# Optimization experiments

Hardware: AMD Instinct MI355X
Metric: run time of the kernel (lower is better)

The kernel has to match this reference:

```python
import jax, jax.numpy as jnp
import numpy as np

B, CIN, COUT, H, W = 32, 64, 64, 58, 58
RSIZE, NB, EDIM = 512, 10, 64


def setup_inputs() -> dict:
    key = jax.random.key(0)
    ks = jax.random.split(key, 8)
    return {
        "x": jax.random.normal(ks[0], (B, CIN, H, W), jnp.float32),
        "routing_vector": jax.random.normal(ks[1], (B, RSIZE), jnp.float32),
        "W1": jax.random.normal(ks[2], (RSIZE, 128), jnp.float32) * 0.02,
        "b1": jnp.zeros((128,), jnp.float32),
        "W2": jax.random.normal(ks[3], (128, EDIM), jnp.float32) * 0.05,
        "b2": jnp.zeros((EDIM,), jnp.float32),
        "emb": jax.random.normal(ks[4], (NB, EDIM), jnp.float32),
        "conv_w": jax.random.normal(ks[5], (NB, COUT, CIN, 3, 3), jnp.float32) * 0.02,
        "conv_b": jnp.zeros((NB, COUT), jnp.float32),
    }


def _cosine_similarity(a, b):
    # calculate_similarity assumed cosine: [B,E] x [N,E] -> [B,N]
    a = a / (jnp.linalg.norm(a, axis=-1, keepdims=True) + 1e-8)
    b = b / (jnp.linalg.norm(b, axis=-1, keepdims=True) + 1e-8)
    return a @ b.T


def reference(x, routing_vector, W1, b1, W2, b2, emb, conv_w, conv_b):
    # process_routing: Linear(512,128) -> ReLU -> Linear(128,64)
    r = jax.nn.relu(routing_vector @ W1 + b1) @ W2 + b2          # [B, 64]
    sim = _cosine_similarity(r, emb)                              # [B, NB]
    # eval mode: no noise; SIMPLESampler treated as identity on softmax weights
    weights = jax.nn.softmax(sim, axis=-1)                        # [B, NB]
    # run all NB expert convs as one valid 3x3 conv with NB*COUT output channels
    w_all = conv_w.reshape(NB * COUT, CIN, 3, 3)
    y = jax.lax.conv_general_dilated(
        x, w_all, window_strides=(1, 1), padding='VALID',
        dimension_numbers=('NCHW', 'OIHW', 'NCHW'))               # [B, NB*COUT, 56, 56]
    y = y + conv_b.reshape(1, NB * COUT, 1, 1)
    y = y.reshape(B, NB, COUT, y.shape[-2], y.shape[-1])          # [B, NB, COUT, 56, 56]
    # weighted mixture over experts; softmax weights sum to 1 (d in torch code)
    d = jnp.sum(weights, axis=-1)                                 # [B]
    out = jnp.einsum('bnchw,bn->bchw', y, weights) / d[:, None, None, None]
    return out
```

## Files before the change

### kernel.cpp

```cpp
#include <hip/hip_runtime.h>
#include <hip/hip_bf16.h>
#include <stdint.h>

#define BATCH 32
#define CIN   64
#define COUT  64
#define HIN   58
#define WIN   58
#define HOUT  56
#define WOUT  56
#define RSIZE 512
#define NB    10
#define EDIM  64
#define HID   128
#define CHW   (HIN*WIN)
#define OHW   (HOUT*WOUT)

typedef __attribute__((ext_vector_type(8)))  short short8;
typedef __attribute__((ext_vector_type(16))) float f32x16;

__device__ __forceinline__ unsigned short f2bf(float f) {
    unsigned int u = __builtin_bit_cast(unsigned int, f);
    u += 0x7fffu + ((u >> 16) & 1u);
    return (unsigned short)(u >> 16);
}

__global__ __launch_bounds__(512) void route_kernel(
    const float* __restrict__ rv, const float* __restrict__ W1,
    const float* __restrict__ b1, const float* __restrict__ W2,
    const float* __restrict__ b2, const float* __restrict__ emb,
    float* __restrict__ wts)
{
    const int b = blockIdx.x;
    const int t = threadIdx.x;

    __shared__ float s_rv[RSIZE];
    __shared__ float s_part[4 * HID];
    __shared__ float s_h[HID];
    __shared__ float s_r[EDIM];
    __shared__ float s_rn;
    __shared__ float s_sim[NB];

    if (t < 128) ((float4*)s_rv)[t] = ((const float4*)(rv + (size_t)b * RSIZE))[t];
    __syncthreads();

    {
        const int h = t & 127, kq = t >> 7;
        float acc = 0.0f;
        const float* wp = W1 + (size_t)(kq * 128) * HID + h;
        const float* xp = s_rv + kq * 128;
        #pragma unroll 8
        for (int k = 0; k < 128; ++k) acc = fmaf(xp[k], wp[(size_t)k * HID], acc);
        s_part[kq * HID + h] = acc;
    }
    __syncthreads();
    if (t < HID)
        s_h[t] = fmaxf(s_part[t] + s_part[HID + t] + s_part[2 * HID + t] +
                       s_part[3 * HID + t] + b1[t], 0.0f);
    __syncthreads();

    {
        const int e = t & 63, kq = t >> 6;
        float acc = 0.0f;
        const float* wp = W2 + (size_t)(kq * 16) * EDIM + e;
        const float* hp = s_h + kq * 16;
        #pragma unroll
        for (int k = 0; k < 16; ++k) acc = fmaf(hp[k], wp[(size_t)k * EDIM], acc);
        s_part[kq * 64 + e] = acc;
    }
    __syncthreads();
    if (t < EDIM) {
        float r = b2[t];
        #pragma unroll
        for (int q = 0; q < 8; ++q) r += s_part[q * 64 + t];
        s_r[t] = r;
    }
    __syncthreads();

    if (t < 64) {
        float sq = s_r[t] * s_r[t];
        #pragma unroll
        for (int off = 32; off; off >>= 1) sq += __shfl_xor(sq, off);
        if (t == 0) s_rn = sqrtf(sq);
    }
    __syncthreads();

    {
        const int wid = t >> 6, lane = t & 63;
        for (int n = wid; n < NB; n += 8) {
            const float ev = emb[n * EDIM + lane];
            float dot = ev * s_r[lane];
            float nb2 = ev * ev;
            #pragma unroll
            for (int off = 32; off; off >>= 1) {
                dot += __shfl_xor(dot, off);
                nb2 += __shfl_xor(nb2, off);
            }
            if (lane == 0)
                s_sim[n] = dot / ((s_rn + 1e-8f) * (sqrtf(nb2) + 1e-8f));
        }
    }
    __syncthreads();

    if (t == 0) {
        float m = -1e30f;
        #pragma unroll
        for (int n = 0; n < NB; ++n) m = fmaxf(m, s_sim[n]);
        float w[NB], sum = 0.0f;
        #pragma unroll
        for (int n = 0; n < NB; ++n) { w[n] = __expf(s_sim[n] - m); sum += w[n]; }
        const float inv = 1.0f / sum;
        float d = 0.0f;
        #pragma unroll
        for (int n = 0; n < NB; ++n) { w[n] *= inv; d += w[n]; }
        const float invd = 1.0f / d;
        #pragma unroll
        for (int n = 0; n < NB; ++n) wts[b * NB + n] = w[n] * invd;
    }
}

__global__ __launch_bounds__(256) void wmix2_kernel(
    const float* __restrict__ cw, const float* __restrict__ cbias,
    const float* __restrict__ wts,
    unsigned short* __restrict__ weffb, float* __restrict__ sbias_g)
{
    const int co = blockIdx.x & 63;
    const int bq = blockIdx.x >> 6;
    const int t  = threadIdx.x;

    __shared__ float scw[NB * 576];
    __shared__ float s_w[8 * NB];

    if (t < 8 * NB) s_w[t] = wts[bq * 8 * NB + t];
    for (int i = t; i < 1440; i += 256) {
        const int n = i / 144, r4 = i - n * 144;
        ((float4*)scw)[(size_t)n * 144 + r4] =
            *(const float4*)(cw + (size_t)(n * COUT + co) * 576 + r4 * 4);
    }
    __syncthreads();

    for (int i = t; i < 8 * 576; i += 256) {
        const int bl  = i / 576, rem = i - bl * 576;
        const int s   = rem >> 6, cin = rem & 63;
        float v = 0.0f;
        #pragma unroll
        for (int n = 0; n < NB; ++n)
            v = fmaf(s_w[bl * NB + n], scw[n * 576 + cin * 9 + s], v);
        const int b  = bq * 8 + bl;
        const int ks = cin >> 4, kg = (cin >> 3) & 1, c8 = cin & 7;
        weffb[((((size_t)(b * 9 + s) * 4 + ks) * 2 + kg) * 64 + co) * 8 + c8] = f2bf(v);
    }
    if (t < 8) {
        float v = 0.0f;
        #pragma unroll
        for (int n = 0; n < NB; ++n) v = fmaf(s_w[t * NB + n], cbias[n * COUT + co], v);
        sbias_g[(bq * 8 + t) * COUT + co] = v;
    }
}

__global__ __launch_bounds__(256, 2) void conv4_kernel(
    const float* __restrict__ x, const unsigned short* __restrict__ weffb,
    const float* __restrict__ sbias_g, float* __restrict__ out)
{
    const int bid  = blockIdx.x;
    const int xcd  = bid & 7;
    const int slot = bid >> 3;
    const int b    = xcd + 8 * (slot / 28);
    const int tile = slot - (slot / 28) * 28;
    const int oh0  = tile * 2;

    const int t    = threadIdx.x;
    const int wid  = t >> 6;
    const int lane = t & 63;
    const int ln   = lane & 31;
    const int kg   = lane >> 5;
    const int mt   = wid & 1;
    const int nh   = wid >> 1;

    __shared__ unsigned short xs[232 * 64];
    __shared__ float sbias[COUT];

    if (t < COUT) sbias[t] = sbias_g[b * COUT + t];

    const float* xg = x + (size_t)b * CIN * CHW + oh0 * WIN;
    #pragma unroll
    for (int k = 0; k < 8; ++k) {
        const int e = t + 256 * k;
        if (e < 1856) {
            const int cb = e / 232;
            const int sp = e - cb * 232;
            const float* gp = xg + (size_t)(cb * 8) * CHW + sp;
            short8 v;
            #pragma unroll
            for (int j = 0; j < 8; ++j)
                v[j] = (short)f2bf(gp[(size_t)j * CHW]);
            *(short8*)&xs[sp * 64 + (cb ^ (sp & 7)) * 8] = v;
        }
    }
    __syncthreads();

    int sbase[2]; int pq[2]; bool val[2];
    #pragma unroll
    for (int nt = 0; nt < 2; ++nt) {
        const int p = (nh * 2 + nt) * 32 + ln;
        val[nt] = (p < 112);
        const int pc = val[nt] ? p : 111;
        pq[nt] = pc;
        const int r = pc / 56, ow = pc - r * 56;
        sbase[nt] = r * WIN + ow;
    }

    f32x16 acc[2];
    #pragma unroll
    for (int nt = 0; nt < 2; ++nt)
        #pragma unroll
        for (int j = 0; j < 16; ++j) acc[nt][j] = 0.0f;

    const unsigned short* abase =
        weffb + (size_t)b * 36864 + kg * 512 + (mt * 32 + ln) * 8;

    #pragma unroll
    for (int ks = 0; ks < 4; ++ks) {
        short8 af[9];
        #pragma unroll
        for (int s = 0; s < 9; ++s)
            af[s] = *(const short8*)(abase + (size_t)s * 4096 + ks * 1024);

        #pragma unroll
        for (int s = 0; s < 9; ++s) {
            const int kh = s / 3, kw = s - kh * 3;
            const int off = kh * WIN + kw;
            #pragma unroll
            for (int nt = 0; nt < 2; ++nt) {
                const int sp   = sbase[nt] + off;
                const int addr = (sp << 7) + ((((ks << 1) + kg) ^ (sp & 7)) << 4);
                const short8 bf = *(const short8*)((const char*)xs + addr);
                acc[nt] = __builtin_amdgcn_mfma_f32_32x32x16_bf16(af[s], bf, acc[nt], 0, 0, 0);
            }
        }
    }

    #pragma unroll
    for (int nt = 0; nt < 2; ++nt) {
        if (!val[nt]) continue;
        const int p = pq[nt];
        const int r = p / 56, ow = p - r * 56;
        float* op = out + ((size_t)(b * COUT + mt * 32) * HOUT + oh0 + r) * WOUT + ow;
        #pragma unroll
        for (int reg = 0; reg < 16; ++reg) {
            const int co_l = (reg & 3) + 8 * (reg >> 2) + 4 * kg;
            op[(size_t)co_l * OHW] = acc[nt][reg] + sbias[mt * 32 + co_l];
        }
    }
}

extern "C" void kernel_launch(void* const* d_in, const int* in_sizes, int n_in,
                              void* d_out, int out_size, void* d_ws, size_t ws_size,
                              hipStream_t stream) {
    const float* x    = (const float*)d_in[0];
    const float* rv   = (const float*)d_in[1];
    const float* W1   = (const float*)d_in[2];
    const float* b1   = (const float*)d_in[3];
    const float* W2   = (const float*)d_in[4];
    const float* b2   = (const float*)d_in[5];
    const float* emb  = (const float*)d_in[6];
    const float* cw   = (const float*)d_in[7];
    const float* cb   = (const float*)d_in[8];
    float* out = (float*)d_out;

    float* wts            = (float*)d_ws;
    float* sbias_g        = (float*)d_ws + 1024;
    unsigned short* weffb = (unsigned short*)((float*)d_ws + 3072);

    route_kernel<<<dim3(BATCH), dim3(512), 0, stream>>>(rv, W1, b1, W2, b2, emb, wts);
    wmix2_kernel<<<dim3(256), dim3(256), 0, stream>>>(cw, cb, wts, weffb, sbias_g);
    conv4_kernel<<<dim3(BATCH * 28), dim3(256), 0, stream>>>(x, weffb, sbias_g, out);
}
```

Baseline: 39.54 us.

## Split conv input staging into two channel halves and use direct-to-LDS loads in weight mix

The conv kernel now stages the input tile in two 32-channel halves with a smaller LDS buffer and a new swizzle, and raises the occupancy hint to 4 blocks per SM. This is meant to let more blocks run at once and hide global load latency. The cost is an extra barrier phase, and the input staging is now serialized with the MFMA work within each block. The weight-mix kernel switches to 512 threads and uses global_load_lds to copy conv weights straight into LDS, avoiding the register round trip.

```diff
diff --git a/kernel.cpp b/kernel.cpp
--- a/kernel.cpp
+++ b/kernel.cpp
@@ -119,7 +119,7 @@
     }
 }
 
-__global__ __launch_bounds__(256) void wmix2_kernel(
+__global__ __launch_bounds__(512) void wmix2b_kernel(
     const float* __restrict__ cw, const float* __restrict__ cbias,
     const float* __restrict__ wts,
     unsigned short* __restrict__ weffb, float* __restrict__ sbias_g)
@@ -132,14 +132,25 @@
     __shared__ float s_w[8 * NB];
 
     if (t < 8 * NB) s_w[t] = wts[bq * 8 * NB + t];
-    for (int i = t; i < 1440; i += 256) {
-        const int n = i / 144, r4 = i - n * 144;
-        ((float4*)scw)[(size_t)n * 144 + r4] =
-            *(const float4*)(cw + (size_t)(n * COUT + co) * 576 + r4 * 4);
-    }
-    __syncthreads();
-
-    for (int i = t; i < 8 * 576; i += 256) {
+
+    {
+        const float* base = cw + (size_t)co * 576;
+        #pragma unroll
+        for (int rnd = 0; rnd < 3; ++rnd) {
+            const int i = t + 512 * rnd;
+            if (i < 1440) {
+                const int n = i / 144, r4 = i - n * 144;
+                __builtin_amdgcn_global_load_lds(
+                    (const __attribute__((address_space(1))) void*)
+                        (base + (size_t)n * (COUT * 576) + r4 * 4),
+                    (__attribute__((address_space(3))) void*)(scw + (size_t)i * 4),
+                    16, 0, 0);
+            }
+        }
+    }
+    __syncthreads();
+
+    for (int i = t; i < 8 * 576; i += 512) {
         const int bl  = i / 576, rem = i - bl * 576;
         const int s   = rem >> 6, cin = rem & 63;
         float v = 0.0f;
@@ -158,7 +169,7 @@
     }
 }
 
-__global__ __launch_bounds__(256, 2) void conv4_kernel(
+__global__ __launch_bounds__(256, 4) void conv5_kernel(
     const float* __restrict__ x, const unsigned short* __restrict__ weffb,
     const float* __restrict__ sbias_g, float* __restrict__ out)
 {
@@ -177,27 +188,10 @@
     const int mt   = wid & 1;
     const int nh   = wid >> 1;
 
-    __shared__ unsigned short xs[232 * 64];
+    __shared__ unsigned short xs[232 * 32];
     __shared__ float sbias[COUT];
 
     if (t < COUT) sbias[t] = sbias_g[b * COUT + t];
-
-    const float* xg = x + (size_t)b * CIN * CHW + oh0 * WIN;
-    #pragma unroll
-    for (int k = 0; k < 8; ++k) {
-        const int e = t + 256 * k;
-        if (e < 1856) {
-            const int cb = e / 232;
-            const int sp = e - cb * 232;
-            const float* gp = xg + (size_t)(cb * 8) * CHW + sp;
-            short8 v;
-            #pragma unroll
-            for (int j = 0; j < 8; ++j)
-                v[j] = (short)f2bf(gp[(size_t)j * CHW]);
-            *(short8*)&xs[sp * 64 + (cb ^ (sp & 7)) * 8] = v;
-        }
-    }
-    __syncthreads();
 
     int sbase[2]; int pq[2]; bool val[2];
     #pragma unroll
@@ -216,26 +210,52 @@
         #pragma unroll
         for (int j = 0; j < 16; ++j) acc[nt][j] = 0.0f;
 
+    const float* xg = x + (size_t)b * CIN * CHW + oh0 * WIN;
     const unsigned short* abase =
         weffb + (size_t)b * 36864 + kg * 512 + (mt * 32 + ln) * 8;
 
     #pragma unroll
-    for (int ks = 0; ks < 4; ++ks) {
-        short8 af[9];
-        #pragma unroll
-        for (int s = 0; s < 9; ++s)
-            af[s] = *(const short8*)(abase + (size_t)s * 4096 + ks * 1024);
-
-        #pragma unroll
-        for (int s = 0; s < 9; ++s) {
-            const int kh = s / 3, kw = s - kh * 3;
-            const int off = kh * WIN + kw;
+    for (int cc = 0; cc < 2; ++cc) {
+        __syncthreads();
+        const float* xg_c = xg + (size_t)(cc * 32) * CHW;
+        #pragma unroll
+        for (int k = 0; k < 4; ++k) {
+            const int e = t + 256 * k;
+            if (e < 928) {
+                const int cb = e / 232;
+                const int sp = e - cb * 232;
+                const float* gp = xg_c + (size_t)(cb * 8) * CHW + sp;
+                short8 v;
+                #pragma unroll
+                for (int j = 0; j < 8; ++j)
+                    v[j] = (short)f2bf(gp[(size_t)j * CHW]);
+                const int slot8 = (((sp & 1) << 2) | cb) ^ ((sp >> 1) & 7);
+                *(short8*)((char*)xs + (sp >> 1) * 128 + slot8 * 16) = v;
+            }
+        }
+        __syncthreads();
+
+        #pragma unroll
+        for (int k2 = 0; k2 < 2; ++k2) {
+            const int ks = cc * 2 + k2;
+            short8 af[9];
             #pragma unroll
-            for (int nt = 0; nt < 2; ++nt) {
-                const int sp   = sbase[nt] + off;
-                const int addr = (sp << 7) + ((((ks << 1) + kg) ^ (sp & 7)) << 4);
-                const short8 bf = *(const short8*)((const char*)xs + addr);
-                acc[nt] = __builtin_amdgcn_mfma_f32_32x32x16_bf16(af[s], bf, acc[nt], 0, 0, 0);
+            for (int s = 0; s < 9; ++s)
+                af[s] = *(const short8*)(abase + (size_t)s * 4096 + ks * 1024);
+
+            const int cb = k2 * 2 + kg;
+            #pragma unroll
+            for (int s = 0; s < 9; ++s) {
+                const int kh = s / 3, kw = s - kh * 3;
+                const int off = kh * WIN + kw;
+                #pragma unroll
+                for (int nt = 0; nt < 2; ++nt) {
+                    const int sp    = sbase[nt] + off;
+                    const int slot8 = (((sp & 1) << 2) | cb) ^ ((sp >> 1) & 7);
+                    const short8 bf =
+                        *(const short8*)((const char*)xs + (sp >> 1) * 128 + slot8 * 16);
+                    acc[nt] = __builtin_amdgcn_mfma_f32_32x32x16_bf16(af[s], bf, acc[nt], 0, 0, 0);
+                }
             }
         }
     }
@@ -273,6 +293,6 @@
     unsigned short* weffb = (unsigned short*)((float*)d_ws + 3072);
 
     route_kernel<<<dim3(BATCH), dim3(512), 0, stream>>>(rv, W1, b1, W2, b2, emb, wts);
-    wmix2_kernel<<<dim3(256), dim3(256), 0, stream>>>(cw, cb, wts, weffb, sbias_g);
-    conv4_kernel<<<dim3(BATCH * 28), dim3(256), 0, stream>>>(x, weffb, sbias_g, out);
-}
+    wmix2b_kernel<<<dim3(256), dim3(512), 0, stream>>>(cw, cb, wts, weffb, sbias_g);
+    conv5_kernel<<<dim3(BATCH * 28), dim3(256), 0, stream>>>(x, weffb, sbias_g, out);
+}
```

New measurement: 41.07 us. 1.04x slower.

## Fuse routing MLP and expert weight mixing into one kernel

Applied to the files above, without the earlier changes.

Merges the routing kernel and the weight-mixing kernel into a single launch. Each of the 256 blocks recomputes the routing MLP, cosine similarity and softmax for its 8 batch entries, then mixes the expert conv weights for one output channel. This removes one kernel launch and the global round-trip for the routing weights. The cost is redundant work: the MLP for each batch group is recomputed 64 times across blocks, and shared memory use per block grows.

```diff
diff --git a/kernel.cpp b/kernel.cpp
--- a/kernel.cpp
+++ b/kernel.cpp
@@ -25,71 +25,98 @@
     return (unsigned short)(u >> 16);
 }
 
-__global__ __launch_bounds__(512) void route_kernel(
+__global__ __launch_bounds__(512) void rwmix_kernel(
     const float* __restrict__ rv, const float* __restrict__ W1,
     const float* __restrict__ b1, const float* __restrict__ W2,
     const float* __restrict__ b2, const float* __restrict__ emb,
-    float* __restrict__ wts)
+    const float* __restrict__ cw, const float* __restrict__ cbias,
+    unsigned short* __restrict__ weffb, float* __restrict__ sbias_g)
 {
-    const int b = blockIdx.x;
-    const int t = threadIdx.x;
-
-    __shared__ float s_rv[RSIZE];
-    __shared__ float s_part[4 * HID];
-    __shared__ float s_h[HID];
-    __shared__ float s_r[EDIM];
-    __shared__ float s_rn;
-    __shared__ float s_sim[NB];
-
-    if (t < 128) ((float4*)s_rv)[t] = ((const float4*)(rv + (size_t)b * RSIZE))[t];
+    const int co = blockIdx.x & 63;
+    const int bq = blockIdx.x >> 6;
+    const int t  = threadIdx.x;
+    const int lane = t & 63;
+    const int wv   = t >> 6;
+
+    __shared__ float s_rv[8][RSIZE];
+    __shared__ float scw[NB * 576];
+    __shared__ float s_part[4096];
+    __shared__ float s_h[8][HID];
+    __shared__ float s_r[8][EDIM];
+    __shared__ float s_rn[8];
+    __shared__ float s_sim[8][NB];
+    __shared__ float s_w[8][NB];
+
+    for (int i = t; i < 1024; i += 512)
+        ((float4*)&s_rv[0][0])[i] = *(const float4*)(rv + (size_t)bq * 8 * RSIZE + i * 4);
+    for (int i = t; i < 1440; i += 512) {
+        const int n = i / 144, r4 = i - n * 144;
+        ((float4*)scw)[n * 144 + r4] =
+            *(const float4*)(cw + (size_t)(n * COUT + co) * 576 + r4 * 4);
+    }
     __syncthreads();
 
     {
         const int h = t & 127, kq = t >> 7;
-        float acc = 0.0f;
+        float a[8];
+        #pragma unroll
+        for (int bl = 0; bl < 8; ++bl) a[bl] = 0.0f;
         const float* wp = W1 + (size_t)(kq * 128) * HID + h;
-        const float* xp = s_rv + kq * 128;
-        #pragma unroll 8
-        for (int k = 0; k < 128; ++k) acc = fmaf(xp[k], wp[(size_t)k * HID], acc);
-        s_part[kq * HID + h] = acc;
-    }
-    __syncthreads();
-    if (t < HID)
-        s_h[t] = fmaxf(s_part[t] + s_part[HID + t] + s_part[2 * HID + t] +
-                       s_part[3 * HID + t] + b1[t], 0.0f);
+        #pragma unroll 4
+        for (int k = 0; k < 128; ++k) {
+            const float w = wp[(size_t)k * HID];
+            #pragma unroll
+            for (int bl = 0; bl < 8; ++bl)
+                a[bl] = fmaf(s_rv[bl][kq * 128 + k], w, a[bl]);
+        }
+        #pragma unroll
+        for (int bl = 0; bl < 8; ++bl) s_part[kq * 1024 + bl * 128 + h] = a[bl];
+    }
+    __syncthreads();
+
+    #pragma unroll
+    for (int rep = 0; rep < 2; ++rep) {
+        const int o  = t + rep * 512;
+        const int bl = o >> 7, h = o & 127;
+        s_h[bl][h] = fmaxf(s_part[bl * 128 + h] + s_part[1024 + bl * 128 + h] +
+                           s_part[2048 + bl * 128 + h] + s_part[3072 + bl * 128 + h] +
+                           b1[h], 0.0f);
+    }
     __syncthreads();
 
     {
         const int e = t & 63, kq = t >> 6;
-        float acc = 0.0f;
+        float a[8];
+        #pragma unroll
+        for (int bl = 0; bl < 8; ++bl) a[bl] = 0.0f;
         const float* wp = W2 + (size_t)(kq * 16) * EDIM + e;
-        const float* hp = s_h + kq * 16;
-        #pragma unroll
-        for (int k = 0; k < 16; ++k) acc = fmaf(hp[k], wp[(size_t)k * EDIM], acc);
-        s_part[kq * 64 + e] = acc;
-    }
-    __syncthreads();
-    if (t < EDIM) {
-        float r = b2[t];
-        #pragma unroll
-        for (int q = 0; q < 8; ++q) r += s_part[q * 64 + t];
-        s_r[t] = r;
-    }
-    __syncthreads();
-
-    if (t < 64) {
-        float sq = s_r[t] * s_r[t];
+        #pragma unroll
+        for (int k = 0; k < 16; ++k) {
+            const float w = wp[(size_t)k * EDIM];
+            #pragma unroll
+            for (int bl = 0; bl < 8; ++bl)
+                a[bl] = fmaf(s_h[bl][kq * 16 + k], w, a[bl]);
+        }
+        #pragma unroll
+        for (int bl = 0; bl < 8; ++bl) s_part[kq * 512 + bl * 64 + e] = a[bl];
+    }
+    __syncthreads();
+
+    {
+        const int e = lane, bl = wv;
+        float r = b2[e];
+        #pragma unroll
+        for (int q = 0; q < 8; ++q) r += s_part[q * 512 + bl * 64 + e];
+        s_r[bl][e] = r;
+
+        float sq = r * r;
         #pragma unroll
         for (int off = 32; off; off >>= 1) sq += __shfl_xor(sq, off);
-        if (t == 0) s_rn = sqrtf(sq);
-    }
-    __syncthreads();
-
-    {
-        const int wid = t >> 6, lane = t & 63;
-        for (int n = wid; n < NB; n += 8) {
-            const float ev = emb[n * EDIM + lane];
-            float dot = ev * s_r[lane];
+        if (lane == 0) s_rn[bl] = sqrtf(sq);
+
+        for (int n = 0; n < NB; ++n) {
+            const float ev = emb[n * EDIM + e];
+            float dot = ev * r;
             float nb2 = ev * ev;
             #pragma unroll
             for (int off = 32; off; off >>= 1) {
@@ -97,55 +124,35 @@
                 nb2 += __shfl_xor(nb2, off);
             }
             if (lane == 0)
-                s_sim[n] = dot / ((s_rn + 1e-8f) * (sqrtf(nb2) + 1e-8f));
-        }
-    }
-    __syncthreads();
-
-    if (t == 0) {
+                s_sim[bl][n] = dot / ((s_rn[bl] + 1e-8f) * (sqrtf(nb2) + 1e-8f));
+        }
+    }
+    __syncthreads();
+
+    if (t < 8) {
         float m = -1e30f;
         #pragma unroll
-        for (int n = 0; n < NB; ++n) m = fmaxf(m, s_sim[n]);
+        for (int n = 0; n < NB; ++n) m = fmaxf(m, s_sim[t][n]);
         float w[NB], sum = 0.0f;
         #pragma unroll
-        for (int n = 0; n < NB; ++n) { w[n] = __expf(s_sim[n] - m); sum += w[n]; }
+        for (int n = 0; n < NB; ++n) { w[n] = __expf(s_sim[t][n] - m); sum += w[n]; }
         const float inv = 1.0f / sum;
         float d = 0.0f;
         #pragma unroll
         for (int n = 0; n < NB; ++n) { w[n] *= inv; d += w[n]; }
         const float invd = 1.0f / d;
         #pragma unroll
-        for (int n = 0; n < NB; ++n) wts[b * NB + n] = w[n] * invd;
-    }
-}
-
-__global__ __launch_bounds__(256) void wmix2_kernel(
-    const float* __restrict__ cw, const float* __restrict__ cbias,
-    const float* __restrict__ wts,
-    unsigned short* __restrict__ weffb, float* __restrict__ sbias_g)
-{
-    const int co = blockIdx.x & 63;
-    const int bq = blockIdx.x >> 6;
-    const int t  = threadIdx.x;
-
-    __shared__ float scw[NB * 576];
-    __shared__ float s_w[8 * NB];
-
-    if (t < 8 * NB) s_w[t] = wts[bq * 8 * NB + t];
-    for (int i = t; i < 1440; i += 256) {
-        const int n = i / 144, r4 = i - n * 144;
-        ((float4*)scw)[(size_t)n * 144 + r4] =
-            *(const float4*)(cw + (size_t)(n * COUT + co) * 576 + r4 * 4);
-    }
-    __syncthreads();
-
-    for (int i = t; i < 8 * 576; i += 256) {
+        for (int n = 0; n < NB; ++n) s_w[t][n] = w[n] * invd;
+    }
+    __syncthreads();
+
+    for (int i = t; i < 8 * 576; i += 512) {
         const int bl  = i / 576, rem = i - bl * 576;
         const int s   = rem >> 6, cin = rem & 63;
         float v = 0.0f;
         #pragma unroll
         for (int n = 0; n < NB; ++n)
-            v = fmaf(s_w[bl * NB + n], scw[n * 576 + cin * 9 + s], v);
+            v = fmaf(s_w[bl][n], scw[n * 576 + cin * 9 + s], v);
         const int b  = bq * 8 + bl;
         const int ks = cin >> 4, kg = (cin >> 3) & 1, c8 = cin & 7;
         weffb[((((size_t)(b * 9 + s) * 4 + ks) * 2 + kg) * 64 + co) * 8 + c8] = f2bf(v);
@@ -153,7 +160,7 @@
     if (t < 8) {
         float v = 0.0f;
         #pragma unroll
-        for (int n = 0; n < NB; ++n) v = fmaf(s_w[t * NB + n], cbias[n * COUT + co], v);
+        for (int n = 0; n < NB; ++n) v = fmaf(s_w[t][n], cbias[n * COUT + co], v);
         sbias_g[(bq * 8 + t) * COUT + co] = v;
     }
 }
@@ -268,11 +275,11 @@
     const float* cb   = (const float*)d_in[8];
     float* out = (float*)d_out;
 
-    float* wts            = (float*)d_ws;
     float* sbias_g        = (float*)d_ws + 1024;
     unsigned short* weffb = (unsigned short*)((float*)d_ws + 3072);
 
-    route_kernel<<<dim3(BATCH), dim3(512), 0, stream>>>(rv, W1, b1, W2, b2, emb, wts);
-    wmix2_kernel<<<dim3(256), dim3(256), 0, stream>>>(cw, cb, wts, weffb, sbias_g);
-    conv4_kernel<<<dim3(BATCH * 28), dim3(256), 0, stream>>>(x, weffb, sbias_g, out);
-}
+    rwmix_kernel<<<dim3(256), dim3(512), 0, stream>>>(
+        rv, W1, b1, W2, b2, emb, cw, cb, weffb, sbias_g);
+    conv4_kernel<<<dim3(BATCH * 28), dim3(256), 0, stream>>>(
+        x, weffb, sbias_g, out);
+}
```

After: 44.35 us. +12.1%, slower.
